# Kernel tuning notes

Hardware: AMD Instinct MI355X
Metric: run time of the kernel (lower is better)

## Reference

```python
import jax, jax.numpy as jnp
import numpy as np

HEADS = 20
SHIFT = 0.6931471805599453  # style_alignment_score_shift = log(2)
KEY_SCALE = 1.0             # style_alignment_score_scale
EPS = 1e-5


def expand_first(feat, scale=1.0):
    # feat: [B, H, S, D]; broadcast style features (batch items 0 and B//2)
    b = feat.shape[0]
    fs = jnp.stack([feat[0], feat[b // 2]])[:, None]           # [2,1,H,S,D]
    fs = jnp.broadcast_to(fs, (2, b // 2) + feat.shape[1:])    # [2,B/2,H,S,D]
    if scale != 1:
        fs = jnp.concatenate([fs[:, :1], scale * fs[:, 1:]], axis=1)
    return fs.reshape(feat.shape)


def concat_first(feat, scale=1.0):
    # concatenate style features along the sequence axis (-2)
    return jnp.concatenate([feat, expand_first(feat, scale=scale)], axis=-2)


def adain(feat):
    # stats over sequence axis (-2); torch .var() is unbiased (ddof=1)
    mean = feat.mean(axis=-2, keepdims=True)
    std = jnp.sqrt(feat.var(axis=-2, keepdims=True, ddof=1) + EPS)
    sm = expand_first(mean)
    ss = expand_first(std)
    return (feat - mean) / std * ss + sm


def setup_inputs() -> dict:
    key = jax.random.key(0)
    ks = jax.random.split(key, 6)
    B, S, C = 4, 1024, 1280
    sc = 1.0 / np.sqrt(C)
    return {
        "hidden_states": jax.random.normal(ks[0], (B, S, C), jnp.float32),
        "Wq": jax.random.normal(ks[1], (C, C), jnp.float32) * sc,
        "Wk": jax.random.normal(ks[2], (C, C), jnp.float32) * sc,
        "Wv": jax.random.normal(ks[3], (C, C), jnp.float32) * sc,
        "Wo": jax.random.normal(ks[4], (C, C), jnp.float32) * sc,
        "bo": jnp.zeros((C,), jnp.float32),
    }


def reference(hidden_states, Wq, Wk, Wv, Wo, bo):
    B, S, C = hidden_states.shape
    H = HEADS
    hd = C // H
    scale = hd ** -0.5

    def to_heads(t):  # [B,S,C] -> [B,H,S,hd]
        return t.reshape(B, S, H, hd).transpose(0, 2, 1, 3)

    q = to_heads(hidden_states @ Wq.T)
    k = to_heads(hidden_states @ Wk.T)
    v = to_heads(hidden_states @ Wv.T)

    q = adain(q)              # adain_queries
    k = adain(k)              # adain_keys
    # adain_values = False

    k = concat_first(k, scale=KEY_SCALE)   # [B,H,2S,hd]
    v = concat_first(v)                    # [B,H,2S,hd]

    # shifted scaled dot-product attention (shift added to shared-key block)
    logits = jnp.einsum('bhqd,bhkd->bhqk', q, k) * scale  # [B,H,S,2S]
    bias = jnp.where(jnp.arange(k.shape[-2]) >= S, jnp.float32(SHIFT), jnp.float32(0.0))
    probs = jax.nn.softmax(logits + bias, axis=-1)
    out = jnp.einsum('bhqk,bhkd->bhqd', probs, v)         # [B,H,S,hd]

    out = out.transpose(0, 2, 1, 3).reshape(B, S, C)
    out = out @ Wo.T + bo
    return out
```

## Files before the change

### kernel.cpp

```cpp
#include <hip/hip_runtime.h>
#include <math.h>


typedef __bf16 bf16x8 __attribute__((ext_vector_type(8)));
typedef float f32x4 __attribute__((ext_vector_type(4)));
typedef unsigned short u16x8 __attribute__((ext_vector_type(8)));

#define BDIM 256

__device__ inline unsigned short f2bf(float f) {
  unsigned int u = __float_as_uint(f);
  u += 0x7fffu + ((u >> 16) & 1u);
  return (unsigned short)(u >> 16);
}
__device__ inline unsigned int pack_bf2(float lo, float hi) {
  return (unsigned int)f2bf(lo) | ((unsigned int)f2bf(hi) << 16);
}
__device__ inline float bf2f(unsigned short h) {
  return __uint_as_float(((unsigned int)h) << 16);
}

__device__ inline void gl_lds16(const unsigned short* g, unsigned short* l) {
  __builtin_amdgcn_global_load_lds(
      (const __attribute__((address_space(1))) unsigned int*)g,
      (__attribute__((address_space(3))) unsigned int*)l, 16, 0, 0);
}

__global__ __launch_bounds__(BDIM) void k_convert_all(
    const float* __restrict__ X, const float* __restrict__ Wq,
    const float* __restrict__ Wk, const float* __restrict__ Wv,
    const float* __restrict__ Wo, unsigned short* __restrict__ Xbf,
    unsigned short* __restrict__ Wcat, unsigned short* __restrict__ Wobf) {
  const int idx = blockIdx.x * BDIM + threadIdx.x;
  const float* src;
  unsigned short* dst;
  int off;
  if (idx < 1310720) {
    src = X; dst = Xbf; off = idx;
  } else {
    const int r = idx - 1310720;
    const int which = r / 409600;
    off = r - which * 409600;
    src = (which == 0) ? Wq : (which == 1) ? Wk : (which == 2) ? Wv : Wo;
    dst = (which < 3) ? Wcat + (size_t)which * 1638400 : Wobf;
  }
  const float4 v = ((const float4*)src)[off];
  ushort4 o;
  o.x = f2bf(v.x); o.y = f2bf(v.y); o.z = f2bf(v.z); o.w = f2bf(v.w);
  ((ushort4*)dst)[off] = o;
}

__global__ __launch_bounds__(BDIM) void k_gemm_bf16(
    const unsigned short* __restrict__ A, const unsigned short* __restrict__ B,
    unsigned short* __restrict__ Cbf, int M, int N, int K) {
  __shared__ unsigned short As[2][128 * 32];
  __shared__ unsigned short Bs[2][128 * 32];
  const int t = threadIdx.x;
  const int w = t >> 6, lane = t & 63, quad = lane >> 4, l16 = lane & 15;
  const int wm = (w >> 1) << 6, wn = (w & 1) << 6;
  const int mBase = blockIdx.x * 128, nBase = blockIdx.y * 128;

  f32x4 acc[4][4];
#pragma unroll
  for (int i = 0; i < 4; i++)
#pragma unroll
    for (int j = 0; j < 4; j++) acc[i][j] = (f32x4){0.f, 0.f, 0.f, 0.f};

  const int r0 = t >> 2;
  const int kk0 = (t & 3) * 8;

  for (int k0 = 0; k0 < K; k0 += 64) {
    const unsigned short* Ab = A + (size_t)(mBase + r0) * K + k0 + kk0;
    const unsigned short* Bb = B + (size_t)(nBase + r0) * K + k0 + kk0;
    gl_lds16(Ab, As[0] + t * 8);
    gl_lds16(Ab + (size_t)64 * K, As[0] + (t + 256) * 8);
    gl_lds16(Ab + 32, As[1] + t * 8);
    gl_lds16(Ab + (size_t)64 * K + 32, As[1] + (t + 256) * 8);
    gl_lds16(Bb, Bs[0] + t * 8);
    gl_lds16(Bb + (size_t)64 * K, Bs[0] + (t + 256) * 8);
    gl_lds16(Bb + 32, Bs[1] + t * 8);
    gl_lds16(Bb + (size_t)64 * K + 32, Bs[1] + (t + 256) * 8);
    __syncthreads();
    bf16x8 af[2][4], bfr[2][4];
#pragma unroll
    for (int hh = 0; hh < 2; hh++)
#pragma unroll
      for (int i = 0; i < 4; i++) {
        af[hh][i] = *(const bf16x8*)(As[hh] + (wm + i * 16 + l16) * 32 + quad * 8);
        bfr[hh][i] = *(const bf16x8*)(Bs[hh] + (wn + i * 16 + l16) * 32 + quad * 8);
      }
#pragma unroll
    for (int hh = 0; hh < 2; hh++)
#pragma unroll
      for (int mi = 0; mi < 4; mi++)
#pragma unroll
        for (int ni = 0; ni < 4; ni++)
          acc[mi][ni] = __builtin_amdgcn_mfma_f32_16x16x32_bf16(
              af[hh][mi], bfr[hh][ni], acc[mi][ni], 0, 0, 0);
    __syncthreads();
  }

#pragma unroll
  for (int mi = 0; mi < 4; mi++)
#pragma unroll
    for (int r = 0; r < 4; r++) {
      const int row = mBase + wm + mi * 16 + quad * 4 + r;
#pragma unroll
      for (int ni = 0; ni < 4; ni++)
        Cbf[(size_t)row * N + nBase + wn + ni * 16 + l16] = f2bf(acc[mi][ni][r]);
    }
}

__global__ __launch_bounds__(BDIM) void k_gemm_64x128(
    const unsigned short* __restrict__ A, const unsigned short* __restrict__ B,
    float* __restrict__ Cf, const float* __restrict__ bias, int M, int N,
    int K) {
  __shared__ unsigned short As[2][64 * 32];
  __shared__ unsigned short Bs[2][128 * 32];
  const int t = threadIdx.x;
  const int w = t >> 6, lane = t & 63, quad = lane >> 4, l16 = lane & 15;
  const int wm = (w >> 1) << 5, wn = (w & 1) << 6;
  const int mBase = blockIdx.x * 64, nBase = blockIdx.y * 128;

  f32x4 acc[2][4];
#pragma unroll
  for (int i = 0; i < 2; i++)
#pragma unroll
    for (int j = 0; j < 4; j++) acc[i][j] = (f32x4){0.f, 0.f, 0.f, 0.f};

  const int r0 = t >> 2;
  const int kk0 = (t & 3) * 8;

  for (int k0 = 0; k0 < K; k0 += 64) {
    const unsigned short* Ab = A + (size_t)(mBase + r0) * K + k0 + kk0;
    const unsigned short* Bb = B + (size_t)(nBase + r0) * K + k0 + kk0;
    gl_lds16(Ab, As[0] + t * 8);
    gl_lds16(Ab + 32, As[1] + t * 8);
    gl_lds16(Bb, Bs[0] + t * 8);
    gl_lds16(Bb + (size_t)64 * K, Bs[0] + (t + 256) * 8);
    gl_lds16(Bb + 32, Bs[1] + t * 8);
    gl_lds16(Bb + (size_t)64 * K + 32, Bs[1] + (t + 256) * 8);
    __syncthreads();
    bf16x8 af[2][2], bfr[2][4];
#pragma unroll
    for (int hh = 0; hh < 2; hh++) {
#pragma unroll
      for (int i = 0; i < 2; i++)
        af[hh][i] = *(const bf16x8*)(As[hh] + (wm + i * 16 + l16) * 32 + quad * 8);
#pragma unroll
      for (int i = 0; i < 4; i++)
        bfr[hh][i] = *(const bf16x8*)(Bs[hh] + (wn + i * 16 + l16) * 32 + quad * 8);
    }
#pragma unroll
    for (int hh = 0; hh < 2; hh++)
#pragma unroll
      for (int mi = 0; mi < 2; mi++)
#pragma unroll
        for (int ni = 0; ni < 4; ni++)
          acc[mi][ni] = __builtin_amdgcn_mfma_f32_16x16x32_bf16(
              af[hh][mi], bfr[hh][ni], acc[mi][ni], 0, 0, 0);
    __syncthreads();
  }

#pragma unroll
  for (int mi = 0; mi < 2; mi++)
#pragma unroll
    for (int r = 0; r < 4; r++) {
      const int row = mBase + wm + mi * 16 + quad * 4 + r;
#pragma unroll
      for (int ni = 0; ni < 4; ni++) {
        const int col = nBase + wn + ni * 16 + l16;
        Cf[(size_t)row * N + col] = acc[mi][ni][r] + bias[col];
      }
    }
}

__global__ __launch_bounds__(320) void k_stats1(
    const unsigned short* __restrict__ QKV, float* __restrict__ psum,
    float* __restrict__ psq) {
  const int z = blockIdx.y, which = z >> 2, b = z & 3;
  const int c = threadIdx.x * 4;
  const size_t base =
      (size_t)(b * 1024 + blockIdx.x * 32) * 3840 + which * 1280 + c;
  float4 s = {0.f, 0.f, 0.f, 0.f}, s2 = {0.f, 0.f, 0.f, 0.f};
#pragma unroll 8
  for (int i = 0; i < 32; ++i) {
    const ushort4 xv = *(const ushort4*)(QKV + base + (size_t)i * 3840);
    const float x0 = bf2f(xv.x), x1 = bf2f(xv.y), x2 = bf2f(xv.z),
                x3 = bf2f(xv.w);
    s.x += x0; s.y += x1; s.z += x2; s.w += x3;
    s2.x = fmaf(x0, x0, s2.x); s2.y = fmaf(x1, x1, s2.y);
    s2.z = fmaf(x2, x2, s2.z); s2.w = fmaf(x3, x3, s2.w);
  }
  const size_t o = ((size_t)z * 32 + blockIdx.x) * 1280 + c;
  *(float4*)(psum + o) = s;
  *(float4*)(psq + o) = s2;
}

__global__ __launch_bounds__(BDIM) void k_stats2(
    const float* __restrict__ psum, const float* __restrict__ psq,
    float* __restrict__ stats) {
  const int z = blockIdx.y, which = z >> 2, b = z & 3;
  const int c = blockIdx.x * 256 + threadIdx.x;
  float s = 0.f, s2 = 0.f;
#pragma unroll
  for (int j = 0; j < 32; ++j) {
    s += psum[((size_t)z * 32 + j) * 1280 + c];
    s2 += psq[((size_t)z * 32 + j) * 1280 + c];
  }
  const float mean = s * (1.0f / 1024.0f);
  const float var = (s2 - 1024.0f * mean * mean) * (1.0f / 1023.0f);
  stats[((which * 2 + 0) * 4 + b) * 1280 + c] = mean;
  stats[((which * 2 + 1) * 4 + b) * 1280 + c] = sqrtf(var + 1e-5f);
}

__global__ __launch_bounds__(BDIM) void k_adain_vt(
    const unsigned short* __restrict__ QKV, const float* __restrict__ stats,
    unsigned short* __restrict__ qn, unsigned short* __restrict__ kn,
    unsigned short* __restrict__ vt) {
  __shared__ unsigned short tile[64][65];
  const int bx = blockIdx.x;
  if (bx < 10240) {
    const int which = bx / 5120;
    const int rem = bx - which * 5120;
    const int b = rem / 1280;
    const int xb = rem - b * 1280;
    const int idx = xb * BDIM + threadIdx.x;
    const int s = idx / 320;
    const int c = (idx - s * 320) * 4;
    const int sb = (b < 2) ? 0 : 2;
    const ushort4 xv = *(const ushort4*)(QKV + ((size_t)(b * 1024 + s)) * 3840 +
                                         which * 1280 + c);
    const float4 mean =
        *(const float4*)(stats + ((which * 2 + 0) * 4 + b) * 1280 + c);
    const float4 stdv =
        *(const float4*)(stats + ((which * 2 + 1) * 4 + b) * 1280 + c);
    const float4 meanS =
        *(const float4*)(stats + ((which * 2 + 0) * 4 + sb) * 1280 + c);
    const float4 stdS =
        *(const float4*)(stats + ((which * 2 + 1) * 4 + sb) * 1280 + c);
    ushort4 o;
    o.x = f2bf((bf2f(xv.x) - mean.x) / stdv.x * stdS.x + meanS.x);
    o.y = f2bf((bf2f(xv.y) - mean.y) / stdv.y * stdS.y + meanS.y);
    o.z = f2bf((bf2f(xv.z) - mean.z) / stdv.z * stdS.z + meanS.z);
    o.w = f2bf((bf2f(xv.w) - mean.w) / stdv.w * stdS.w + meanS.w);
    unsigned short* dst = (which == 0) ? qn : kn;
    *(ushort4*)(dst + ((size_t)(b * 1024 + s)) * 1280 + c) = o;
  } else {
    const int tb = bx - 10240;
    const int b = tb / 320;
    const int r2 = tb - b * 320;
    const int c0 = (r2 / 16) * 64;
    const int s0 = (r2 & 15) * 64;
    const int t = threadIdx.x;
    const int r = t >> 2, seg = (t & 3) * 16;
    const size_t goff = ((size_t)(b * 1024 + s0 + r)) * 3840 + 2560 + c0 + seg;
    const u16x8 va = *(const u16x8*)(QKV + goff);
    const u16x8 vb = *(const u16x8*)(QKV + goff + 8);
#pragma unroll
    for (int j = 0; j < 8; j++) {
      tile[r][seg + j] = va[j];
      tile[r][seg + 8 + j] = vb[j];
    }
    __syncthreads();
    u16x8 o0, o1;
#pragma unroll
    for (int j = 0; j < 8; j++) {
      o0[j] = tile[seg + j][r];
      o1[j] = tile[seg + 8 + j][r];
    }
    const size_t ooff = ((size_t)(b * 1280 + c0 + r)) * 1024 + s0 + seg;
    *(u16x8*)(vt + ooff) = o0;
    *(u16x8*)(vt + ooff + 8) = o1;
  }
}

__global__ __launch_bounds__(BDIM, 3) void k_attn(
    const unsigned short* __restrict__ qn, const unsigned short* __restrict__ kn,
    const unsigned short* __restrict__ vt, unsigned short* __restrict__ Opart,
    float* __restrict__ Lpart) {
  const int S = 1024, C = 1280;
  const int qt = blockIdx.x, h = blockIdx.y, zs = blockIdx.z;
  int b, chunk;
  if (zs < 2)      { b = 0; chunk = zs; }
  else if (zs < 6) { b = 1; chunk = zs - 2; }
  else if (zs < 8) { b = 2; chunk = zs - 6; }
  else             { b = 3; chunk = zs - 8; }
  const int ktBeg = chunk * 8;
  const int t = threadIdx.x, w = t >> 6, lane = t & 63;
  const int quad = lane >> 4, l16 = lane & 15;
  const int bstyle = (b < 2) ? 0 : 2;
  const int qrow = qt * 128 + w * 32;

  __shared__ unsigned short Ks[2][2][64 * 32];
  __shared__ unsigned short Vs[2][2][64 * 32];
  __shared__ unsigned short Plds[4][32][64];

  bf16x8 aq[2][2];
#pragma unroll
  for (int g = 0; g < 2; ++g) {
    const size_t qoff =
        ((size_t)(b * S + qrow + g * 16 + l16)) * C + h * 64 + quad * 8;
    aq[g][0] = *(const bf16x8*)(qn + qoff);
    aq[g][1] = *(const bf16x8*)(qn + qoff + 32);
  }

  bf16x8 ones;
#pragma unroll
  for (int i = 0; i < 8; ++i) ones[i] = (__bf16)1.0f;

  f32x4 o[2][4], lsum[2];
#pragma unroll
  for (int g = 0; g < 2; ++g) {
    lsum[g] = (f32x4){0.f, 0.f, 0.f, 0.f};
#pragma unroll
    for (int i = 0; i < 4; i++) o[g][i] = (f32x4){0.f, 0.f, 0.f, 0.f};
  }

  const int krow = t >> 2;
  const int kseg = (t & 3) * 8;
  const int sw = l16 & 14;

  auto stage = [&](int buf, int kt) {
    const int bs = (kt < 16) ? b : bstyle;
    const int sk = (kt & 15) * 64;
    const unsigned short* kg =
        kn + (size_t)(bs * S + sk + krow) * C + h * 64 + kseg;
    gl_lds16(kg, Ks[buf][0] + t * 8);
    gl_lds16(kg + 32, Ks[buf][1] + t * 8);
    const unsigned short* vg =
        vt + (size_t)(bs * C + h * 64 + krow) * S + sk + kseg;
    gl_lds16(vg, Vs[buf][0] + t * 8);
    gl_lds16(vg + 32, Vs[buf][1] + t * 8);
  };

  stage(0, ktBeg);

  const float SCALE2 = 0.125f * 1.44269504088896341f;

  for (int i = 0; i < 8; ++i) {
    const int kt = ktBeg + i;
    const int buf = i & 1;
    __syncthreads();
    if (i + 1 < 8) stage(buf ^ 1, kt + 1);

    const float bias2 = (kt >= 16) ? 1.0f : 0.0f;

    f32x4 z2[2][4];
#pragma unroll
    for (int nt = 0; nt < 4; ++nt) {
      const bf16x8 bk0 =
          *(const bf16x8*)(Ks[buf][0] + (nt * 16 + l16) * 32 + quad * 8);
      const bf16x8 bk1 =
          *(const bf16x8*)(Ks[buf][1] + (nt * 16 + l16) * 32 + quad * 8);
#pragma unroll
      for (int g = 0; g < 2; ++g) {
        f32x4 zz = (f32x4){0.f, 0.f, 0.f, 0.f};
        zz = __builtin_amdgcn_mfma_f32_16x16x32_bf16(bk0, aq[g][0], zz, 0, 0, 0);
        zz = __builtin_amdgcn_mfma_f32_16x16x32_bf16(bk1, aq[g][1], zz, 0, 0, 0);
        z2[g][nt] = zz;
      }
    }

#pragma unroll
    for (int g = 0; g < 2; ++g) {
#pragma unroll
      for (int nt = 0; nt < 4; ++nt) {
        const float e0 = exp2f(fmaf(z2[g][nt][0], SCALE2, bias2));
        const float e1 = exp2f(fmaf(z2[g][nt][1], SCALE2, bias2));
        const float e2 = exp2f(fmaf(z2[g][nt][2], SCALE2, bias2));
        const float e3 = exp2f(fmaf(z2[g][nt][3], SCALE2, bias2));
        uint2 pk;
        pk.x = pack_bf2(e0, e1);
        pk.y = pack_bf2(e2, e3);
        const int phys = (nt * 4 + quad) ^ sw;
        *(uint2*)(&Plds[w][g * 16 + l16][phys * 4]) = pk;
      }
    }

#pragma unroll
    for (int g = 0; g < 2; ++g) {
      const int a0 = (2 * quad) ^ sw;
      const int a1 = (2 * quad + 8) ^ sw;
      const bf16x8 pa0 = *(const bf16x8*)(&Plds[w][g * 16 + l16][a0 * 4]);
      const bf16x8 pa1 = *(const bf16x8*)(&Plds[w][g * 16 + l16][a1 * 4]);
      lsum[g] = __builtin_amdgcn_mfma_f32_16x16x32_bf16(pa0, ones, lsum[g], 0, 0, 0);
      lsum[g] = __builtin_amdgcn_mfma_f32_16x16x32_bf16(pa1, ones, lsum[g], 0, 0, 0);
#pragma unroll
      for (int dt = 0; dt < 4; ++dt) {
        const bf16x8 vb0 =
            *(const bf16x8*)(Vs[buf][0] + (dt * 16 + l16) * 32 + quad * 8);
        const bf16x8 vb1 =
            *(const bf16x8*)(Vs[buf][1] + (dt * 16 + l16) * 32 + quad * 8);
        o[g][dt] =
            __builtin_amdgcn_mfma_f32_16x16x32_bf16(pa0, vb0, o[g][dt], 0, 0, 0);
        o[g][dt] =
            __builtin_amdgcn_mfma_f32_16x16x32_bf16(pa1, vb1, o[g][dt], 0, 0, 0);
      }
    }
  }

  if (l16 == 0) {
#pragma unroll
    for (int g = 0; g < 2; ++g)
#pragma unroll
      for (int r = 0; r < 4; ++r)
        Lpart[((size_t)zs * 20 + h) * 1024 + qrow + g * 16 + quad * 4 + r] =
            lsum[g][r];
  }

  unsigned short* Op = Opart + (size_t)zs * 1024 * 1280;
#pragma unroll
  for (int g = 0; g < 2; ++g)
#pragma unroll
    for (int dt = 0; dt < 4; ++dt)
#pragma unroll
      for (int r = 0; r < 4; ++r)
        Op[(size_t)(qrow + g * 16 + quad * 4 + r) * 1280 + h * 64 + dt * 16 +
           l16] = f2bf(o[g][dt][r]);
}

__global__ __launch_bounds__(BDIM) void k_combine(
    const unsigned short* __restrict__ Opart, const float* __restrict__ Lpart,
    unsigned short* __restrict__ attnb) {
  const int idx = blockIdx.x * BDIM + threadIdx.x;
  const int row = idx / 160;
  const int c = (idx - row * 160) * 8;
  const int b = row >> 10, q = row & 1023, h = c >> 6;
  const int zb = (b >> 1) * 6 + (b & 1) * 2;
  const int ns = 2 + (b & 1) * 2;
  float L = 0.f;
  float acc[8] = {0.f, 0.f, 0.f, 0.f, 0.f, 0.f, 0.f, 0.f};
  for (int s = 0; s < ns; ++s) {
    L += Lpart[((size_t)(zb + s) * 20 + h) * 1024 + q];
    const u16x8 v =
        *(const u16x8*)(Opart + (size_t)(zb + s) * 1310720 + (size_t)q * 1280 + c);
#pragma unroll
    for (int j = 0; j < 8; ++j) acc[j] += bf2f(v[j]);
  }
  const float rl = 1.0f / L;
  u16x8 o8;
#pragma unroll
  for (int j = 0; j < 8; ++j) o8[j] = f2bf(acc[j] * rl);
  *(u16x8*)(attnb + (size_t)row * 1280 + c) = o8;
}

extern "C" void kernel_launch(void* const* d_in, const int* in_sizes, int n_in,
                              void* d_out, int out_size, void* d_ws,
                              size_t ws_size, hipStream_t stream) {
  const float* X = (const float*)d_in[0];
  const float* Wq = (const float*)d_in[1];
  const float* Wk = (const float*)d_in[2];
  const float* Wv = (const float*)d_in[3];
  const float* Wo = (const float*)d_in[4];
  const float* bo = (const float*)d_in[5];
  float* out = (float*)d_out;

  char* ws = (char*)d_ws;
  size_t off = 0;
  auto alloc = [&](size_t bytes) {
    char* p = ws + off;
    off += (bytes + 255) & ~(size_t)255;
    return p;
  };
  unsigned short* Wcat = (unsigned short*)alloc(3840ull * 1280 * 2);
  unsigned short* Xbf = (unsigned short*)alloc(4096ull * 1280 * 2);
  unsigned short* QKV = (unsigned short*)alloc(4096ull * 3840 * 2);
  unsigned short* Wobf = (unsigned short*)alloc(1280ull * 1280 * 2);
  float* stats = (float*)alloc(2ull * 2 * 4 * 1280 * 4);
  unsigned short* qnb = (unsigned short*)alloc(4096ull * 1280 * 2);
  unsigned short* knb = (unsigned short*)alloc(4096ull * 1280 * 2);
  unsigned short* vtb = (unsigned short*)alloc(4096ull * 1280 * 2);
  unsigned short* attnb = (unsigned short*)alloc(4096ull * 1280 * 2);

  unsigned short* Opart = QKV;
  float* Lpart = (float*)Wcat;
  float* psum = (float*)attnb;
  float* psq = (float*)(attnb + 4096ull * 1280 / 2);

  k_convert_all<<<11520, BDIM, 0, stream>>>(X, Wq, Wk, Wv, Wo, Xbf, Wcat, Wobf);
  k_gemm_bf16<<<dim3(32, 30), BDIM, 0, stream>>>(Xbf, Wcat, QKV, 4096, 3840,
                                                 1280);
  k_stats1<<<dim3(32, 8), 320, 0, stream>>>(QKV, psum, psq);
  k_stats2<<<dim3(5, 8), BDIM, 0, stream>>>(psum, psq, stats);
  k_adain_vt<<<11520, BDIM, 0, stream>>>(QKV, stats, qnb, knb, vtb);
  k_attn<<<dim3(8, 20, 12), BDIM, 0, stream>>>(qnb, knb, vtb, Opart, Lpart);
  k_combine<<<2560, BDIM, 0, stream>>>(Opart, Lpart, attnb);
  k_gemm_64x128<<<dim3(64, 10), BDIM, 0, stream>>>(attnb, Wobf, out, bo, 4096,
                                                   1280, 1280);
}
```

Before: 288.6 us.

## Halve attention key tile to 32 rows to double occupancy

Shrinks the per-iteration key/value tile in the attention kernel from 64 to 32 keys and doubles the iteration count, which halves the LDS footprint for K, V and P. Launch bounds go from 3 to 6 blocks per CU, so more waves can hide latency. The P-tile write/read layout and swizzle are rebuilt for the narrower tile. The cost is twice as many barriers and smaller MFMA batches per sync, which may reduce instruction-level overlap.

```diff
diff --git a/kernel.cpp b/kernel.cpp
--- a/kernel.cpp
+++ b/kernel.cpp
@@ -275,7 +275,7 @@
   }
 }
 
-__global__ __launch_bounds__(BDIM, 3) void k_attn(
+__global__ __launch_bounds__(BDIM, 6) void k_attn(
     const unsigned short* __restrict__ qn, const unsigned short* __restrict__ kn,
     const unsigned short* __restrict__ vt, unsigned short* __restrict__ Opart,
     float* __restrict__ Lpart) {
@@ -286,15 +286,15 @@
   else if (zs < 6) { b = 1; chunk = zs - 2; }
   else if (zs < 8) { b = 2; chunk = zs - 6; }
   else             { b = 3; chunk = zs - 8; }
-  const int ktBeg = chunk * 8;
+  const int itBeg = chunk * 16;
   const int t = threadIdx.x, w = t >> 6, lane = t & 63;
   const int quad = lane >> 4, l16 = lane & 15;
   const int bstyle = (b < 2) ? 0 : 2;
   const int qrow = qt * 128 + w * 32;
 
-  __shared__ unsigned short Ks[2][2][64 * 32];
-  __shared__ unsigned short Vs[2][2][64 * 32];
-  __shared__ unsigned short Plds[4][32][64];
+  __shared__ unsigned short Ks[2][2048];
+  __shared__ unsigned short Vs[2][2048];
+  __shared__ unsigned short Plds[4][32][32];
 
   bf16x8 aq[2][2];
 #pragma unroll
@@ -317,42 +317,39 @@
     for (int i = 0; i < 4; i++) o[g][i] = (f32x4){0.f, 0.f, 0.f, 0.f};
   }
 
-  const int krow = t >> 2;
-  const int kseg = (t & 3) * 8;
-  const int sw = l16 & 14;
-
-  auto stage = [&](int buf, int kt) {
-    const int bs = (kt < 16) ? b : bstyle;
-    const int sk = (kt & 15) * 64;
-    const unsigned short* kg =
-        kn + (size_t)(bs * S + sk + krow) * C + h * 64 + kseg;
-    gl_lds16(kg, Ks[buf][0] + t * 8);
-    gl_lds16(kg + 32, Ks[buf][1] + t * 8);
-    const unsigned short* vg =
-        vt + (size_t)(bs * C + h * 64 + krow) * S + sk + kseg;
-    gl_lds16(vg, Vs[buf][0] + t * 8);
-    gl_lds16(vg + 32, Vs[buf][1] + t * 8);
+  const int kr = (t & 127) >> 2;
+  const int kc = (t & 3) * 8 + (t >> 7) * 32;
+  const int vr = t >> 2;
+  const int vc = (t & 3) * 8;
+
+  auto stage = [&](int buf, int it) {
+    const int bs = (it < 32) ? b : bstyle;
+    const int sk = (it & 31) * 32;
+    gl_lds16(kn + (size_t)(bs * S + sk + kr) * C + h * 64 + kc, Ks[buf] + t * 8);
+    gl_lds16(vt + (size_t)(bs * C + h * 64 + vr) * S + sk + vc, Vs[buf] + t * 8);
   };
 
-  stage(0, ktBeg);
+  stage(0, itBeg);
 
   const float SCALE2 = 0.125f * 1.44269504088896341f;
-
-  for (int i = 0; i < 8; ++i) {
-    const int kt = ktBeg + i;
+  const int swz = l16 & 3;
+  const int h_ = quad >> 1;
+  const int qw0 = (2 * quad) & 3, qw1 = (2 * quad + 1) & 3;
+
+  for (int i = 0; i < 16; ++i) {
+    const int it = itBeg + i;
     const int buf = i & 1;
     __syncthreads();
-    if (i + 1 < 8) stage(buf ^ 1, kt + 1);
-
-    const float bias2 = (kt >= 16) ? 1.0f : 0.0f;
-
-    f32x4 z2[2][4];
-#pragma unroll
-    for (int nt = 0; nt < 4; ++nt) {
-      const bf16x8 bk0 =
-          *(const bf16x8*)(Ks[buf][0] + (nt * 16 + l16) * 32 + quad * 8);
+    if (i + 1 < 16) stage(buf ^ 1, it + 1);
+
+    const float bias2 = (it >= 32) ? 1.0f : 0.0f;
+
+    f32x4 z2[2][2];
+#pragma unroll
+    for (int nt = 0; nt < 2; ++nt) {
+      const bf16x8 bk0 = *(const bf16x8*)(Ks[buf] + (nt * 16 + l16) * 32 + quad * 8);
       const bf16x8 bk1 =
-          *(const bf16x8*)(Ks[buf][1] + (nt * 16 + l16) * 32 + quad * 8);
+          *(const bf16x8*)(Ks[buf] + 1024 + (nt * 16 + l16) * 32 + quad * 8);
 #pragma unroll
       for (int g = 0; g < 2; ++g) {
         f32x4 zz = (f32x4){0.f, 0.f, 0.f, 0.f};
@@ -364,38 +361,42 @@
 
 #pragma unroll
     for (int g = 0; g < 2; ++g) {
-#pragma unroll
-      for (int nt = 0; nt < 4; ++nt) {
-        const float e0 = exp2f(fmaf(z2[g][nt][0], SCALE2, bias2));
-        const float e1 = exp2f(fmaf(z2[g][nt][1], SCALE2, bias2));
-        const float e2 = exp2f(fmaf(z2[g][nt][2], SCALE2, bias2));
-        const float e3 = exp2f(fmaf(z2[g][nt][3], SCALE2, bias2));
-        uint2 pk;
+      uint4 pk;
+      {
+        const float e0 = exp2f(fmaf(z2[g][0][0], SCALE2, bias2));
+        const float e1 = exp2f(fmaf(z2[g][0][1], SCALE2, bias2));
+        const float e2 = exp2f(fmaf(z2[g][0][2], SCALE2, bias2));
+        const float e3 = exp2f(fmaf(z2[g][0][3], SCALE2, bias2));
         pk.x = pack_bf2(e0, e1);
         pk.y = pack_bf2(e2, e3);
-        const int phys = (nt * 4 + quad) ^ sw;
-        *(uint2*)(&Plds[w][g * 16 + l16][phys * 4]) = pk;
-      }
+      }
+      {
+        const float e0 = exp2f(fmaf(z2[g][1][0], SCALE2, bias2));
+        const float e1 = exp2f(fmaf(z2[g][1][1], SCALE2, bias2));
+        const float e2 = exp2f(fmaf(z2[g][1][2], SCALE2, bias2));
+        const float e3 = exp2f(fmaf(z2[g][1][3], SCALE2, bias2));
+        pk.z = pack_bf2(e0, e1);
+        pk.w = pack_bf2(e2, e3);
+      }
+      *(uint4*)(&Plds[w][g * 16 + l16][(quad ^ swz) * 8]) = pk;
     }
 
 #pragma unroll
     for (int g = 0; g < 2; ++g) {
-      const int a0 = (2 * quad) ^ sw;
-      const int a1 = (2 * quad + 8) ^ sw;
-      const bf16x8 pa0 = *(const bf16x8*)(&Plds[w][g * 16 + l16][a0 * 4]);
-      const bf16x8 pa1 = *(const bf16x8*)(&Plds[w][g * 16 + l16][a1 * 4]);
-      lsum[g] = __builtin_amdgcn_mfma_f32_16x16x32_bf16(pa0, ones, lsum[g], 0, 0, 0);
-      lsum[g] = __builtin_amdgcn_mfma_f32_16x16x32_bf16(pa1, ones, lsum[g], 0, 0, 0);
+      const uint2 lo =
+          *(const uint2*)(&Plds[w][g * 16 + l16][(qw0 ^ swz) * 8 + h_ * 4]);
+      const uint2 hi =
+          *(const uint2*)(&Plds[w][g * 16 + l16][(qw1 ^ swz) * 8 + h_ * 4]);
+      union { unsigned int u[4]; bf16x8 v; } pu;
+      pu.u[0] = lo.x; pu.u[1] = lo.y; pu.u[2] = hi.x; pu.u[3] = hi.y;
+      const bf16x8 pa = pu.v;
+      lsum[g] = __builtin_amdgcn_mfma_f32_16x16x32_bf16(pa, ones, lsum[g], 0, 0, 0);
 #pragma unroll
       for (int dt = 0; dt < 4; ++dt) {
-        const bf16x8 vb0 =
-            *(const bf16x8*)(Vs[buf][0] + (dt * 16 + l16) * 32 + quad * 8);
-        const bf16x8 vb1 =
-            *(const bf16x8*)(Vs[buf][1] + (dt * 16 + l16) * 32 + quad * 8);
+        const bf16x8 vb =
+            *(const bf16x8*)(Vs[buf] + (dt * 16 + l16) * 32 + quad * 8);
         o[g][dt] =
-            __builtin_amdgcn_mfma_f32_16x16x32_bf16(pa0, vb0, o[g][dt], 0, 0, 0);
-        o[g][dt] =
-            __builtin_amdgcn_mfma_f32_16x16x32_bf16(pa1, vb1, o[g][dt], 0, 0, 0);
+            __builtin_amdgcn_mfma_f32_16x16x32_bf16(pa, vb, o[g][dt], 0, 0, 0);
       }
     }
   }
```

Result: slower. 424.7 us (+47.1%).

## Shrink attention LDS footprint to raise occupancy, single-buffer V and halve P tile

Applied to the files above, without the earlier changes.

The attention kernel now single-buffers V in LDS and loads it at the start of each iteration instead of prefetching it. It halves the P staging tile by processing the probability block in two 32-column chunks, with wider 16-byte writes and a new swizzle. Launch bounds go from 3 to 5 blocks per SM so that the smaller LDS footprint allows more resident waves. The cost is a second __syncthreads per iteration and a V load that is no longer hidden behind the previous iteration, plus a tighter register budget.

```diff
diff --git a/kernel.cpp b/kernel.cpp
--- a/kernel.cpp
+++ b/kernel.cpp
@@ -275,7 +275,7 @@
   }
 }
 
-__global__ __launch_bounds__(BDIM, 3) void k_attn(
+__global__ __launch_bounds__(BDIM, 5) void k_attn(
     const unsigned short* __restrict__ qn, const unsigned short* __restrict__ kn,
     const unsigned short* __restrict__ vt, unsigned short* __restrict__ Opart,
     float* __restrict__ Lpart) {
@@ -293,8 +293,8 @@
   const int qrow = qt * 128 + w * 32;
 
   __shared__ unsigned short Ks[2][2][64 * 32];
-  __shared__ unsigned short Vs[2][2][64 * 32];
-  __shared__ unsigned short Plds[4][32][64];
+  __shared__ unsigned short Vs[2][64 * 32];
+  __shared__ unsigned short Plds[4][32][32];
 
   bf16x8 aq[2][2];
 #pragma unroll
@@ -319,30 +319,37 @@
 
   const int krow = t >> 2;
   const int kseg = (t & 3) * 8;
-  const int sw = l16 & 14;
-
-  auto stage = [&](int buf, int kt) {
+
+  auto stageK = [&](int buf, int kt) {
     const int bs = (kt < 16) ? b : bstyle;
     const int sk = (kt & 15) * 64;
     const unsigned short* kg =
         kn + (size_t)(bs * S + sk + krow) * C + h * 64 + kseg;
     gl_lds16(kg, Ks[buf][0] + t * 8);
     gl_lds16(kg + 32, Ks[buf][1] + t * 8);
+  };
+  auto stageV = [&](int kt) {
+    const int bs = (kt < 16) ? b : bstyle;
+    const int sk = (kt & 15) * 64;
     const unsigned short* vg =
         vt + (size_t)(bs * C + h * 64 + krow) * S + sk + kseg;
-    gl_lds16(vg, Vs[buf][0] + t * 8);
-    gl_lds16(vg + 32, Vs[buf][1] + t * 8);
+    gl_lds16(vg, Vs[0] + t * 8);
+    gl_lds16(vg + 32, Vs[1] + t * 8);
   };
 
-  stage(0, ktBeg);
+  stageK(0, ktBeg);
 
   const float SCALE2 = 0.125f * 1.44269504088896341f;
+  const int swz = l16 & 3;
+  const int h_ = quad >> 1;
+  const int qw0 = (2 * quad) & 3, qw1 = (2 * quad + 1) & 3;
 
   for (int i = 0; i < 8; ++i) {
     const int kt = ktBeg + i;
     const int buf = i & 1;
     __syncthreads();
-    if (i + 1 < 8) stage(buf ^ 1, kt + 1);
+    stageV(kt);
+    if (i + 1 < 8) stageK(buf ^ 1, kt + 1);
 
     const float bias2 = (kt >= 16) ? 1.0f : 0.0f;
 
@@ -362,42 +369,57 @@
       }
     }
 
-#pragma unroll
-    for (int g = 0; g < 2; ++g) {
-#pragma unroll
-      for (int nt = 0; nt < 4; ++nt) {
-        const float e0 = exp2f(fmaf(z2[g][nt][0], SCALE2, bias2));
-        const float e1 = exp2f(fmaf(z2[g][nt][1], SCALE2, bias2));
-        const float e2 = exp2f(fmaf(z2[g][nt][2], SCALE2, bias2));
-        const float e3 = exp2f(fmaf(z2[g][nt][3], SCALE2, bias2));
-        uint2 pk;
-        pk.x = pack_bf2(e0, e1);
-        pk.y = pack_bf2(e2, e3);
-        const int phys = (nt * 4 + quad) ^ sw;
-        *(uint2*)(&Plds[w][g * 16 + l16][phys * 4]) = pk;
+    bf16x8 pa[2][2];
+#pragma unroll
+    for (int c = 0; c < 2; ++c) {
+#pragma unroll
+      for (int g = 0; g < 2; ++g) {
+        uint4 pk;
+        {
+          const float e0 = exp2f(fmaf(z2[g][2 * c][0], SCALE2, bias2));
+          const float e1 = exp2f(fmaf(z2[g][2 * c][1], SCALE2, bias2));
+          const float e2 = exp2f(fmaf(z2[g][2 * c][2], SCALE2, bias2));
+          const float e3 = exp2f(fmaf(z2[g][2 * c][3], SCALE2, bias2));
+          pk.x = pack_bf2(e0, e1);
+          pk.y = pack_bf2(e2, e3);
+        }
+        {
+          const float e0 = exp2f(fmaf(z2[g][2 * c + 1][0], SCALE2, bias2));
+          const float e1 = exp2f(fmaf(z2[g][2 * c + 1][1], SCALE2, bias2));
+          const float e2 = exp2f(fmaf(z2[g][2 * c + 1][2], SCALE2, bias2));
+          const float e3 = exp2f(fmaf(z2[g][2 * c + 1][3], SCALE2, bias2));
+          pk.z = pack_bf2(e0, e1);
+          pk.w = pack_bf2(e2, e3);
+        }
+        *(uint4*)(&Plds[w][g * 16 + l16][(quad ^ swz) * 8]) = pk;
       }
-    }
-
-#pragma unroll
-    for (int g = 0; g < 2; ++g) {
-      const int a0 = (2 * quad) ^ sw;
-      const int a1 = (2 * quad + 8) ^ sw;
-      const bf16x8 pa0 = *(const bf16x8*)(&Plds[w][g * 16 + l16][a0 * 4]);
-      const bf16x8 pa1 = *(const bf16x8*)(&Plds[w][g * 16 + l16][a1 * 4]);
-      lsum[g] = __builtin_amdgcn_mfma_f32_16x16x32_bf16(pa0, ones, lsum[g], 0, 0, 0);
-      lsum[g] = __builtin_amdgcn_mfma_f32_16x16x32_bf16(pa1, ones, lsum[g], 0, 0, 0);
-#pragma unroll
-      for (int dt = 0; dt < 4; ++dt) {
-        const bf16x8 vb0 =
-            *(const bf16x8*)(Vs[buf][0] + (dt * 16 + l16) * 32 + quad * 8);
-        const bf16x8 vb1 =
-            *(const bf16x8*)(Vs[buf][1] + (dt * 16 + l16) * 32 + quad * 8);
-        o[g][dt] =
-            __builtin_amdgcn_mfma_f32_16x16x32_bf16(pa0, vb0, o[g][dt], 0, 0, 0);
-        o[g][dt] =
-            __builtin_amdgcn_mfma_f32_16x16x32_bf16(pa1, vb1, o[g][dt], 0, 0, 0);
+#pragma unroll
+      for (int g = 0; g < 2; ++g) {
+        const uint2 lo =
+            *(const uint2*)(&Plds[w][g * 16 + l16][(qw0 ^ swz) * 8 + h_ * 4]);
+        const uint2 hi =
+            *(const uint2*)(&Plds[w][g * 16 + l16][(qw1 ^ swz) * 8 + h_ * 4]);
+        union { unsigned int u[4]; bf16x8 v; } pu;
+        pu.u[0] = lo.x; pu.u[1] = lo.y; pu.u[2] = hi.x; pu.u[3] = hi.y;
+        pa[g][c] = pu.v;
+        lsum[g] = __builtin_amdgcn_mfma_f32_16x16x32_bf16(pa[g][c], ones,
+                                                          lsum[g], 0, 0, 0);
       }
     }
+
+    __syncthreads();
+
+#pragma unroll
+    for (int c = 0; c < 2; ++c)
+#pragma unroll
+      for (int g = 0; g < 2; ++g)
+#pragma unroll
+        for (int dt = 0; dt < 4; ++dt) {
+          const bf16x8 vb =
+              *(const bf16x8*)(Vs[c] + (dt * 16 + l16) * 32 + quad * 8);
+          o[g][dt] = __builtin_amdgcn_mfma_f32_16x16x32_bf16(pa[g][c], vb,
+                                                             o[g][dt], 0, 0, 0);
+        }
   }
 
   if (l16 == 0) {
```

New measurement: 323.3 us. +12.0%, slower.
